# Kernel tuning notes

Hardware: AMD Instinct MI355X
Metric: run time of the kernel (lower is better)

Reference implementation:

```python
import jax, jax.numpy as jnp
import numpy as np

B, N, M = 4, 4096, 4096  # samples, pred pts/sample, target pts/sample
LOSS_WEIGHT = 1.0


def setup_inputs() -> dict:
    key = jax.random.key(0)
    k1, k2, k3 = jax.random.split(key, 3)
    pred_pc = jax.random.normal(k1, (B * N, 3), dtype=jnp.float32)
    target = jax.random.normal(k2, (B * M, 3), dtype=jnp.float32)
    label = jax.random.randint(k3, (B * N,), 0, 2)  # binary keep-mask per pred point
    nums = jnp.full((B,), N, dtype=jnp.int32)        # uniform ragged sizes (static for jit)
    dense_nums = jnp.full((B,), M, dtype=jnp.int32)
    return {"pred_pc": pred_pc, "target": target, "label": label,
            "nums": nums, "dense_nums": dense_nums}


def reference(pred_pc, target, label, nums, dense_nums):
    b = nums.shape[0]
    p = pred_pc.reshape(b, -1, 3)      # [B,N,3]
    t = target.reshape(b, -1, 3)       # [B,M,3]
    mask = (label.reshape(b, -1) == 1) # [B,N] valid pred points

    # squared pairwise distances via |p|^2 + |t|^2 - 2 p.t  -> [B,N,M]
    pn = jnp.sum(p * p, axis=-1)
    tn = jnp.sum(t * t, axis=-1)
    d = pn[:, :, None] + tn[:, None, :] - 2.0 * jnp.einsum('bnd,bmd->bnm', p, t)
    d = jnp.maximum(d, 0.0)

    # pred -> target: min over M, L1 (sqrt before mean), masked mean over valid preds
    d1 = jnp.sqrt(jnp.min(d, axis=2))                              # [B,N]
    cnt = jnp.maximum(jnp.sum(mask, axis=1), 1)
    m1 = jnp.sum(jnp.where(mask, d1, 0.0), axis=1) / cnt           # [B]

    # target -> pred: min over valid pred points only (invalid rows masked to +big)
    BIG = jnp.float32(1e10)
    d2 = jnp.sqrt(jnp.min(jnp.where(mask[:, :, None], d, BIG), axis=1))  # [B,M]
    m2 = jnp.mean(d2, axis=1)                                      # [B]

    per_sample = 0.5 * (m1 + m2)   # ChamferDistanceL1: (d1.mean()+d2.mean())/2
    return jnp.mean(per_sample) * LOSS_WEIGHT
```

## Files before the change

### kernel.cpp

```cpp
#include <hip/hip_runtime.h>

#define TPB   256
#define QPT   16
#define SPLIT 128
#define RTPB  256
#define QCHUNK 64

__global__ void __launch_bounds__(TPB) nn_kernel(
    const float* __restrict__ pred,
    const float* __restrict__ target,
    const int*   __restrict__ label,
    float* __restrict__ minsplit,
    int B, int N, int M, int natmax, int stride)
{
    __shared__ float4 tile[TPB];

    const int dir = blockIdx.z;
    const float* __restrict__ A  = dir ? target : pred;
    const float* __restrict__ Bp = dir ? pred   : target;
    const int NA = dir ? M : N;
    const int NB = dir ? N : M;
    const int* __restrict__ labB = dir ? label : nullptr;

    const int natiles = (NA + TPB * QPT - 1) / (TPB * QPT);
    const int b  = blockIdx.x / natmax;
    const int at = blockIdx.x - b * natmax;
    if (at >= natiles) return;

    const size_t abase = (size_t)b * NA;

    float px[QPT], py[QPT], pz[QPT], pn[QPT], best[QPT];
#pragma unroll
    for (int q = 0; q < QPT; ++q) {
        int a = at * (TPB * QPT) + q * TPB + threadIdx.x;
        int idx = (a < NA) ? a : 0;
        const float* sp = A + (abase + idx) * 3;
        px[q] = sp[0];
        py[q] = sp[1];
        pz[q] = sp[2];
        pn[q] = fmaf(px[q], px[q], fmaf(py[q], py[q], pz[q] * pz[q]));
        best[q] = 3.0e38f;
    }

    const int slen = (NB + SPLIT - 1) / SPLIT;
    const int sbeg = blockIdx.y * slen;
    const int send = min(sbeg + slen, NB);
    const size_t bbase = (size_t)b * NB;

    for (int c = sbeg; c < send; c += TPB) {
        const int cnt = min(send - c, TPB);
        if (threadIdx.x < cnt) {
            int m = c + threadIdx.x;
            const float* sp = Bp + (bbase + m) * 3;
            float x = sp[0], y = sp[1], z = sp[2];
            float tn = fmaf(x, x, fmaf(y, y, z * z));
            if (labB != nullptr && labB[bbase + m] != 1) {
                x = 0.0f; y = 0.0f; z = 0.0f; tn = 1.0e10f;
            }
            tile[threadIdx.x] = make_float4(-2.f * x, -2.f * y, -2.f * z, tn);
        }
        __syncthreads();

        const int jeven = cnt & ~1;
#pragma unroll 2
        for (int j = 0; j < jeven; j += 2) {
            float4 t0 = tile[j];
            float4 t1 = tile[j + 1];
#pragma unroll
            for (int q = 0; q < QPT; ++q) {
                float v0 = fmaf(px[q], t0.x, fmaf(py[q], t0.y, fmaf(pz[q], t0.z, t0.w)));
                float v1 = fmaf(px[q], t1.x, fmaf(py[q], t1.y, fmaf(pz[q], t1.z, t1.w)));
                best[q] = fminf(best[q], fminf(v0, v1));
            }
        }
        if (cnt & 1) {
            float4 t0 = tile[cnt - 1];
#pragma unroll
            for (int q = 0; q < QPT; ++q) {
                float v0 = fmaf(px[q], t0.x, fmaf(py[q], t0.y, fmaf(pz[q], t0.z, t0.w)));
                best[q] = fminf(best[q], v0);
            }
        }
        __syncthreads();
    }

    float* out = minsplit + (((size_t)dir * B + b) * SPLIT + blockIdx.y) * stride;
#pragma unroll
    for (int q = 0; q < QPT; ++q) {
        int a = at * (TPB * QPT) + q * TPB + threadIdx.x;
        if (a < NA) {
            out[a] = fmaxf(best[q] + pn[q], 0.0f);
        }
    }
}

__global__ void __launch_bounds__(RTPB) reduce1_kernel(
    const float* __restrict__ minsplit,
    const int* __restrict__ label,
    float* __restrict__ pS, float* __restrict__ pC,
    int B, int N, int M, int chunksN, int chunksM, int stride)
{
    __shared__ float red[RTPB];
    const int r = blockIdx.x;

    int dir, b, ch, NA;
    if (r < B * chunksN) { dir = 0; b = r / chunksN; ch = r - b * chunksN; NA = N; }
    else { int r2 = r - B * chunksN; dir = 1; b = r2 / chunksM; ch = r2 - b * chunksM; NA = M; }

    const int lane = threadIdx.x & 63;
    const int sg   = threadIdx.x >> 6;
    const int q    = ch * QCHUNK + lane;

    const float* base = minsplit + ((size_t)(dir * B + b) * SPLIT) * stride + q;

    float m = 3.0e38f;
    if (q < NA) {
#pragma unroll 8
        for (int sp = sg; sp < SPLIT; sp += 4) {
            m = fminf(m, base[(size_t)sp * stride]);
        }
    }
    red[threadIdx.x] = m;
    __syncthreads();

    if (threadIdx.x < QCHUNK) {
        float mm = fminf(fminf(red[lane], red[64 + lane]),
                         fminf(red[128 + lane], red[192 + lane]));
        float s = 0.0f, cc = 0.0f;
        if (q < NA) {
            if (dir == 0) {
                if (label[(size_t)b * N + q] == 1) { s = sqrtf(mm); cc = 1.0f; }
            } else {
                s = sqrtf(mm);
            }
        }
        for (int off = 32; off > 0; off >>= 1) {
            s  += __shfl_down(s, off);
            cc += __shfl_down(cc, off);
        }
        if (lane == 0) { pS[r] = s; pC[r] = cc; }
    }
}

#define MAXB 64
__global__ void __launch_bounds__(256) final_kernel(
    const float* __restrict__ pS, const float* __restrict__ pC,
    float* __restrict__ out, int B, int M, int chunksN, int chunksM)
{
    __shared__ float S[2 * MAXB], C[2 * MAXB];
    const int wave = threadIdx.x >> 6;
    const int lane = threadIdx.x & 63;

    for (int p = wave; p < 2 * B; p += 4) {
        const int dir = (p >= B);
        const int b   = dir ? (p - B) : p;
        const int nch = dir ? chunksM : chunksN;
        const int off = dir ? (B * chunksN + b * chunksM) : (b * chunksN);
        float s = 0.0f, cc = 0.0f;
        for (int i = lane; i < nch; i += 64) {
            s  += pS[off + i];
            cc += pC[off + i];
        }
        for (int o = 32; o > 0; o >>= 1) {
            s  += __shfl_down(s, o);
            cc += __shfl_down(cc, o);
        }
        if (lane == 0) { S[p] = s; C[p] = cc; }
    }
    __syncthreads();

    if (threadIdx.x == 0) {
        float acc = 0.0f;
        for (int b = 0; b < B; ++b) {
            float m1 = S[b] / fmaxf(C[b], 1.0f);
            float m2 = S[B + b] / (float)M;
            acc += 0.5f * (m1 + m2);
        }
        out[0] = acc / (float)B;
    }
}

extern "C" void kernel_launch(void* const* d_in, const int* in_sizes, int n_in,
                              void* d_out, int out_size, void* d_ws, size_t ws_size,
                              hipStream_t stream) {
    const float* pred   = (const float*)d_in[0];
    const float* target = (const float*)d_in[1];
    const int*   label  = (const int*)  d_in[2];

    const int B = in_sizes[3];
    const int N = in_sizes[2] / B;
    const int M = in_sizes[1] / (3 * B);

    const int stride = (N > M) ? N : M;

    float* minsplit = (float*)d_ws;
    const int chunksN = (N + QCHUNK - 1) / QCHUNK;
    const int chunksM = (M + QCHUNK - 1) / QCHUNK;
    const int nred = B * (chunksN + chunksM);
    float* pS = minsplit + (size_t)2 * B * SPLIT * stride;
    float* pC = pS + nred;

    const int nat1 = (N + TPB * QPT - 1) / (TPB * QPT);
    const int nat2 = (M + TPB * QPT - 1) / (TPB * QPT);
    const int natmax = (nat1 > nat2) ? nat1 : nat2;
    dim3 g(B * natmax, SPLIT, 2);
    nn_kernel<<<g, TPB, 0, stream>>>(pred, target, label, minsplit,
                                     B, N, M, natmax, stride);

    reduce1_kernel<<<nred, RTPB, 0, stream>>>(minsplit, label, pS, pC,
                                              B, N, M, chunksN, chunksM, stride);

    final_kernel<<<1, 256, 0, stream>>>(pS, pC, (float*)d_out,
                                        B, M, chunksN, chunksM);
}
```

Baseline: 36.37 us.

## Fuse final reduction into reduce kernel via last-block counter, retune tiling

Removes the separate single-block final kernel by having each reduce block publish its partials atomically and increment a global counter, with the last block computing the final loss. The counter is reset inside the nn kernel. It also halves queries per thread and the target split count, and raises the inner-loop unroll, which changes the grid shape and per-thread register use. This saves one launch at the cost of a serial tail done by one thread, plus extra atomics.

```diff
diff --git a/kernel.cpp b/kernel.cpp
--- a/kernel.cpp
+++ b/kernel.cpp
@@ -1,19 +1,25 @@
 #include <hip/hip_runtime.h>
 
 #define TPB   256
-#define QPT   16
-#define SPLIT 128
+#define QPT   8
+#define SPLIT 64
 #define RTPB  256
 #define QCHUNK 64
+#define MAXPART 1024
 
 __global__ void __launch_bounds__(TPB) nn_kernel(
     const float* __restrict__ pred,
     const float* __restrict__ target,
     const int*   __restrict__ label,
     float* __restrict__ minsplit,
+    unsigned int* __restrict__ counter,
     int B, int N, int M, int natmax, int stride)
 {
     __shared__ float4 tile[TPB];
+
+    if (blockIdx.x == 0 && blockIdx.y == 0 && blockIdx.z == 0 && threadIdx.x == 0) {
+        *counter = 0u;
+    }
 
     const int dir = blockIdx.z;
     const float* __restrict__ A  = dir ? target : pred;
@@ -62,7 +68,7 @@
         __syncthreads();
 
         const int jeven = cnt & ~1;
-#pragma unroll 2
+#pragma unroll 4
         for (int j = 0; j < jeven; j += 2) {
             float4 t0 = tile[j];
             float4 t1 = tile[j + 1];
@@ -94,11 +100,13 @@
     }
 }
 
-__global__ void __launch_bounds__(RTPB) reduce1_kernel(
+__global__ void __launch_bounds__(RTPB) reduce_kernel(
     const float* __restrict__ minsplit,
     const int* __restrict__ label,
     float* __restrict__ pS, float* __restrict__ pC,
-    int B, int N, int M, int chunksN, int chunksM, int stride)
+    unsigned int* __restrict__ counter,
+    float* __restrict__ out,
+    int B, int N, int M, int chunksN, int chunksM, int stride, int nblocks)
 {
     __shared__ float red[RTPB];
     const int r = blockIdx.x;
@@ -123,10 +131,10 @@
     red[threadIdx.x] = m;
     __syncthreads();
 
+    float s = 0.0f, cc = 0.0f;
     if (threadIdx.x < QCHUNK) {
         float mm = fminf(fminf(red[lane], red[64 + lane]),
                          fminf(red[128 + lane], red[192 + lane]));
-        float s = 0.0f, cc = 0.0f;
         if (q < NA) {
             if (dir == 0) {
                 if (label[(size_t)b * N + q] == 1) { s = sqrtf(mm); cc = 1.0f; }
@@ -138,45 +146,42 @@
             s  += __shfl_down(s, off);
             cc += __shfl_down(cc, off);
         }
-        if (lane == 0) { pS[r] = s; pC[r] = cc; }
-    }
-}
-
-#define MAXB 64
-__global__ void __launch_bounds__(256) final_kernel(
-    const float* __restrict__ pS, const float* __restrict__ pC,
-    float* __restrict__ out, int B, int M, int chunksN, int chunksM)
-{
-    __shared__ float S[2 * MAXB], C[2 * MAXB];
-    const int wave = threadIdx.x >> 6;
-    const int lane = threadIdx.x & 63;
-
-    for (int p = wave; p < 2 * B; p += 4) {
-        const int dir = (p >= B);
-        const int b   = dir ? (p - B) : p;
-        const int nch = dir ? chunksM : chunksN;
-        const int off = dir ? (B * chunksN + b * chunksM) : (b * chunksN);
-        float s = 0.0f, cc = 0.0f;
-        for (int i = lane; i < nch; i += 64) {
-            s  += pS[off + i];
-            cc += pC[off + i];
-        }
-        for (int o = 32; o > 0; o >>= 1) {
-            s  += __shfl_down(s, o);
-            cc += __shfl_down(cc, o);
-        }
-        if (lane == 0) { S[p] = s; C[p] = cc; }
+    }
+
+    __shared__ unsigned int is_last;
+    if (threadIdx.x == 0) {
+        atomicExch(&pS[r], s);
+        atomicExch(&pC[r], cc);
+        __threadfence();
+        unsigned int old = atomicAdd(counter, 1u);
+        is_last = (old == (unsigned int)(nblocks - 1)) ? 1u : 0u;
     }
     __syncthreads();
 
-    if (threadIdx.x == 0) {
-        float acc = 0.0f;
-        for (int b = 0; b < B; ++b) {
-            float m1 = S[b] / fmaxf(C[b], 1.0f);
-            float m2 = S[B + b] / (float)M;
-            acc += 0.5f * (m1 + m2);
-        }
-        out[0] = acc / (float)B;
+    if (is_last) {
+        __shared__ float sS[MAXPART], sC[MAXPART];
+        for (int i = threadIdx.x; i < nblocks; i += RTPB) {
+            sS[i] = atomicAdd(&pS[i], 0.0f);
+            sC[i] = atomicAdd(&pC[i], 0.0f);
+        }
+        __syncthreads();
+        if (threadIdx.x == 0) {
+            float acc = 0.0f;
+            for (int bb = 0; bb < B; ++bb) {
+                float S1 = 0.0f, C1 = 0.0f, S2 = 0.0f;
+                for (int i = 0; i < chunksN; ++i) {
+                    S1 += sS[bb * chunksN + i];
+                    C1 += sC[bb * chunksN + i];
+                }
+                for (int i = 0; i < chunksM; ++i) {
+                    S2 += sS[B * chunksN + bb * chunksM + i];
+                }
+                float m1 = S1 / fmaxf(C1, 1.0f);
+                float m2 = S2 / (float)M;
+                acc += 0.5f * (m1 + m2);
+            }
+            out[0] = acc / (float)B;
+        }
     }
 }
 
@@ -199,17 +204,16 @@
     const int nred = B * (chunksN + chunksM);
     float* pS = minsplit + (size_t)2 * B * SPLIT * stride;
     float* pC = pS + nred;
+    unsigned int* counter = (unsigned int*)(pC + nred);
 
     const int nat1 = (N + TPB * QPT - 1) / (TPB * QPT);
     const int nat2 = (M + TPB * QPT - 1) / (TPB * QPT);
     const int natmax = (nat1 > nat2) ? nat1 : nat2;
     dim3 g(B * natmax, SPLIT, 2);
-    nn_kernel<<<g, TPB, 0, stream>>>(pred, target, label, minsplit,
+    nn_kernel<<<g, TPB, 0, stream>>>(pred, target, label, minsplit, counter,
                                      B, N, M, natmax, stride);
 
-    reduce1_kernel<<<nred, RTPB, 0, stream>>>(minsplit, label, pS, pC,
-                                              B, N, M, chunksN, chunksM, stride);
-
-    final_kernel<<<1, 256, 0, stream>>>(pS, pC, (float*)d_out,
-                                        B, M, chunksN, chunksM);
+    reduce_kernel<<<nred, RTPB, 0, stream>>>(minsplit, label, pS, pC, counter,
+                                             (float*)d_out,
+                                             B, N, M, chunksN, chunksM, stride, nred);
 }
```

Result: slower. 41.98 us (median of 2 runs) (+15.4%).
